# Kernel tuning notes

Measured on AMD Instinct MI355X. Metric: run time of the kernel, lower is better.

Reference implementation:

```python
import jax, jax.numpy as jnp
import numpy as np

D_MODEL = 1024
N_HEADS = 16
D_K = D_MODEL // N_HEADS
D_FF = 4096
EPS = 1e-5


def _linear_params(key, d_in, d_out):
    kw, kb = jax.random.split(key)
    lim = 1.0 / np.sqrt(d_in)
    W = jax.random.uniform(kw, (d_in, d_out), jnp.float32, -lim, lim)
    b = jax.random.uniform(kb, (d_out,), jnp.float32, -lim, lim)
    return W, b


def setup_inputs() -> dict:
    key = jax.random.key(0)
    ks = jax.random.split(key, 8)
    x = jax.random.normal(ks[0], (4, 2048, D_MODEL), jnp.float32)
    wq, bq = _linear_params(ks[1], D_MODEL, D_MODEL)
    wk, bk = _linear_params(ks[2], D_MODEL, D_MODEL)
    wv, bv = _linear_params(ks[3], D_MODEL, D_MODEL)
    wo, bo = _linear_params(ks[4], D_MODEL, D_MODEL)
    w1, b1 = _linear_params(ks[5], D_MODEL, D_FF)
    w2, b2 = _linear_params(ks[6], D_FF, D_MODEL)
    g1 = jnp.ones((D_MODEL,), jnp.float32)
    be1 = jnp.zeros((D_MODEL,), jnp.float32)
    g2 = jnp.ones((D_MODEL,), jnp.float32)
    be2 = jnp.zeros((D_MODEL,), jnp.float32)
    return dict(x=x, wq=wq, bq=bq, wk=wk, bk=bk, wv=wv, bv=bv, wo=wo, bo=bo,
                w1=w1, b1=b1, w2=w2, b2=b2, g1=g1, be1=be1, g2=g2, be2=be2)


def _layernorm(x, gamma, beta):
    mu = jnp.mean(x, axis=-1, keepdims=True)
    var = jnp.mean(jnp.square(x - mu), axis=-1, keepdims=True)
    return (x - mu) * jax.lax.rsqrt(var + EPS) * gamma + beta


def _encoder_layer(x, wq, bq, wk, bk, wv, bv, wo, bo, w1, b1, w2, b2, g1, be1, g2, be2):
    B, S, _ = x.shape
    # QKV projections, split into heads: (B, H, S, d_k)
    def split_heads(t):
        return t.reshape(B, S, N_HEADS, D_K).transpose(0, 2, 1, 3)
    q = split_heads(x @ wq + bq)
    k = split_heads(x @ wk + bk)
    v = split_heads(x @ wv + bv)
    scores = jnp.einsum('bhqd,bhkd->bhqk', q, k) / np.sqrt(D_K).astype(np.float32)
    attn = jax.nn.softmax(scores, axis=-1)
    ctx = jnp.einsum('bhqk,bhkd->bhqd', attn, v)
    ctx = ctx.transpose(0, 2, 1, 3).reshape(B, S, D_MODEL)
    attn_out = ctx @ wo + bo
    x = _layernorm(x + attn_out, g1, be1)
    ff = jax.nn.relu(x @ w1 + b1) @ w2 + b2
    x = _layernorm(x + ff, g2, be2)
    return x


def reference(x, wq, bq, wk, bk, wv, bv, wo, bo, w1, b1, w2, b2, g1, be1, g2, be2):
    return _encoder_layer(x, wq, bq, wk, bk, wv, bv, wo, bo, w1, b1, w2, b2, g1, be1, g2, be2)
```

## Files before the change

### kernel.cpp

```cpp
#include <hip/hip_runtime.h>
#include <hip/hip_bf16.h>

#define DEV __device__ __forceinline__

typedef __attribute__((ext_vector_type(8))) short bf16x8;
typedef __attribute__((ext_vector_type(4))) float f32x4;

constexpr int B = 4, S = 2048, D = 1024, H = 16, DK = 64, DFF = 4096;
constexpr int NT = B * S;
constexpr int HS = B * H * S;
constexpr float QSCALE = 0.125f * 1.44269504088896f;

#if __has_builtin(__builtin_amdgcn_exp2f)
#define EXP2(x) __builtin_amdgcn_exp2f(x)
#else
#define EXP2(x) exp2f(x)
#endif

#define BARRIER()                         \
  asm volatile("" ::: "memory");          \
  __builtin_amdgcn_s_barrier();           \
  asm volatile("" ::: "memory")

DEV unsigned short f2bf(float f) {
  return __builtin_bit_cast(unsigned short, __float2bfloat16(f));
}
DEV float bf2f(unsigned short u) { return __uint_as_float((unsigned)u << 16); }

DEV void gld16(unsigned short* ldsbase, const unsigned short* g, int lane) {
#if __has_builtin(__builtin_amdgcn_global_load_lds)
  __builtin_amdgcn_global_load_lds((const __attribute__((address_space(1))) unsigned int*)g,
                                   (__attribute__((address_space(3))) unsigned int*)ldsbase,
                                   16, 0, 0);
#else
  *(uint4*)(ldsbase + lane * 8) = *(const uint4*)g;
#endif
}

__global__ __launch_bounds__(256) void cvt_bf16_kernel(const float* __restrict__ in,
                                                       unsigned short* __restrict__ out, int n) {
  int i = (blockIdx.x * 256 + threadIdx.x) * 8;
  if (i >= n) return;
  float4 a = *(const float4*)(in + i);
  float4 b = *(const float4*)(in + i + 4);
  uint4 o;
  o.x = f2bf(a.x) | ((unsigned)f2bf(a.y) << 16);
  o.y = f2bf(a.z) | ((unsigned)f2bf(a.w) << 16);
  o.z = f2bf(b.x) | ((unsigned)f2bf(b.y) << 16);
  o.w = f2bf(b.z) | ((unsigned)f2bf(b.w) << 16);
  *(uint4*)(out + i) = o;
}

__global__ __launch_bounds__(256) void transpose_cvt_all_kernel(
    const float* __restrict__ wq, const float* __restrict__ wk, const float* __restrict__ wv,
    const float* __restrict__ wo, const float* __restrict__ w1, const float* __restrict__ w2,
    unsigned short* __restrict__ wqkvT, unsigned short* __restrict__ woT,
    unsigned short* __restrict__ w1T, unsigned short* __restrict__ w2T) {
  __shared__ unsigned short tile[64][72];
  int bid = blockIdx.x;
  const float* in;
  unsigned short* out;
  int R, C, tb;
  if (bid < 1024) {
    int wsel = bid >> 8;
    tb = bid & 255;
    R = 1024; C = 1024;
    in = wsel == 0 ? wq : wsel == 1 ? wk : wsel == 2 ? wv : wo;
    out = wsel < 3 ? wqkvT + (size_t)wsel * D * D : woT;
  } else if (bid < 2048) {
    tb = bid - 1024; R = 1024; C = 4096; in = w1; out = w1T;
  } else {
    tb = bid - 2048; R = 4096; C = 1024; in = w2; out = w2T;
  }
  int gx = C >> 6;
  int rb = (tb / gx) * 64, cb = (tb % gx) * 64;
  int t = threadIdx.x;
#pragma unroll
  for (int i = 0; i < 16; ++i) {
    int c = t + i * 256;
    int r = c >> 6, cc = c & 63;
    tile[cc][r] = f2bf(in[(size_t)(rb + r) * C + cb + cc]);
  }
  __syncthreads();
#pragma unroll
  for (int i = 0; i < 16; ++i) {
    int c = t + i * 256;
    int rr = c >> 6, cc = c & 63;
    out[(size_t)(cb + rr) * R + rb + cc] = tile[rr][cc];
  }
}

template <int BNW, int OMODE, bool RELU>
__global__ __launch_bounds__(512) void gemm256_kernel(const unsigned short* __restrict__ A,
                                                      const unsigned short* __restrict__ WT,
                                                      const float* __restrict__ bias0,
                                                      const float* __restrict__ bias1,
                                                      const float* __restrict__ bias2,
                                                      const unsigned short* __restrict__ res,
                                                      void* __restrict__ out0,
                                                      void* __restrict__ out1,
                                                      void* __restrict__ out2,
                                                      int M, int N, int K) {
  constexpr int BN = BNW * 64;
  __shared__ __align__(16) unsigned short sA[2][2][256 * 32];
  __shared__ __align__(16) unsigned short sB[2][2][BN * 32];

  int t = threadIdx.x, w = t >> 6, l = t & 63;
  int ll = l & 15, lh = l >> 4;

  int lin = blockIdx.x, nwg = gridDim.x;
  int wg = (nwg & 7) == 0 ? (lin & 7) * (nwg >> 3) + (lin >> 3) : lin;
  int gx = N / BN;
  int bn = wg % gx, bm = wg / gx;

  const int wm = (w >> 2) * 128, wn = (w & 3) * (BNW * 16);
  const int ua = (lh ^ ((ll >> 1) & 3)) * 8;

  f32x4 acc[8][BNW] = {};

  const int pr = t >> 2, up = t & 3;
  const int ulog = up ^ ((pr >> 1) & 3);
  const unsigned short* gA0 = A + ((size_t)bm * 256 + pr) * K + ulog * 8;
  const unsigned short* gB0 = WT + ((size_t)bn * BN + pr) * K + ulog * 8;

  auto stgA = [&](int buf, int kh, int tile) {
    const unsigned short* s = gA0 + (size_t)tile * 64 + kh * 32;
    gld16(&sA[buf][kh][w * 512], s, l);
    gld16(&sA[buf][kh][4096 + w * 512], s + (size_t)128 * K, l);
  };
  auto stgB = [&](int buf, int kh, int tile) {
    const unsigned short* s = gB0 + (size_t)tile * 64 + kh * 32;
    gld16(&sB[buf][kh][w * 512], s, l);
    if constexpr (BNW == 4) gld16(&sB[buf][kh][4096 + w * 512], s + (size_t)128 * K, l);
  };

  const int NK = K >> 6;
  stgA(0, 0, 0); stgB(0, 0, 0);
  stgA(0, 1, 0); stgB(0, 1, 0);
  stgA(1, 0, 1); stgB(1, 0, 1);
  if constexpr (BNW == 4) asm volatile("s_waitcnt vmcnt(4)" ::: "memory");
  else                    asm volatile("s_waitcnt vmcnt(3)" ::: "memory");
  BARRIER();

  bf16x8 bfr[BNW];
  for (int it = 0; it < NK; it += 2) {
    const bool more = it + 2 < NK;
#pragma unroll
    for (int ph = 0; ph < 8; ++ph) {
      const int tb = ph >> 2;
      const int kh = (ph >> 1) & 1;
      const int mq = ph & 1;
      bf16x8 af[4];
      if (mq == 0) {
#pragma unroll
        for (int nt = 0; nt < BNW; ++nt)
          bfr[nt] = *(const bf16x8*)(&sB[tb][kh][(wn + nt * 16 + ll) * 32 + ua]);
      }
#pragma unroll
      for (int i = 0; i < 4; ++i)
        af[i] = *(const bf16x8*)(&sA[tb][kh][(wm + (mq * 4 + i) * 16 + ll) * 32 + ua]);
      if (ph == 0) stgA(1, 1, it + 1);
      else if (ph == 1) stgB(1, 1, it + 1);
      else if (more) {
        if (ph == 2) stgA(0, 0, it + 2);
        else if (ph == 3) stgB(0, 0, it + 2);
        else if (ph == 4) stgA(0, 1, it + 2);
        else if (ph == 5) stgB(0, 1, it + 2);
        else if (ph == 6) stgA(1, 0, it + 3);
        else stgB(1, 0, it + 3);
      }
      BARRIER();
      __builtin_amdgcn_s_setprio(1);
#pragma unroll
      for (int i = 0; i < 4; ++i)
#pragma unroll
        for (int nt = 0; nt < BNW; ++nt)
          acc[mq * 4 + i][nt] =
              __builtin_amdgcn_mfma_f32_16x16x32_bf16(af[i], bfr[nt], acc[mq * 4 + i][nt], 0, 0, 0);
      __builtin_amdgcn_s_setprio(0);
      if (ph == 3 || ph == 7) {
        if (more) {
          if constexpr (BNW == 4) asm volatile("s_waitcnt vmcnt(4)" ::: "memory");
          else                    asm volatile("s_waitcnt vmcnt(3)" ::: "memory");
        } else {
          asm volatile("s_waitcnt vmcnt(0)" ::: "memory");
        }
      }
      BARRIER();
    }
  }

#pragma unroll
  for (int mt = 0; mt < 8; ++mt) {
#pragma unroll
    for (int nt = 0; nt < BNW; ++nt) {
      int col = bn * BN + wn + nt * 16 + ll;
      int row0 = bm * 256 + wm + mt * 16 + lh * 4;
      if constexpr (OMODE == 3) {
        int sec = col >> 10, c = col & 1023;
        float bv = (sec == 0 ? bias0 : (sec == 1 ? bias1 : bias2))[c];
        if (sec == 2) {
          int b_ = row0 >> 11, s_ = row0 & 2047;
          size_t vr = ((size_t)(b_ * H + (c >> 6)) * 64 + (c & 63)) * S + s_;
          uint2 pk;
          pk.x = (unsigned)f2bf(acc[mt][nt][0] + bv) | ((unsigned)f2bf(acc[mt][nt][1] + bv) << 16);
          pk.y = (unsigned)f2bf(acc[mt][nt][2] + bv) | ((unsigned)f2bf(acc[mt][nt][3] + bv) << 16);
          *(uint2*)((unsigned short*)out2 + vr) = pk;
        } else {
          unsigned short* o = sec == 0 ? (unsigned short*)out0 : (unsigned short*)out1;
          float sc_ = sec == 0 ? QSCALE : 1.f;
#pragma unroll
          for (int r = 0; r < 4; ++r)
            o[(size_t)(row0 + r) * 1024 + c] = f2bf((acc[mt][nt][r] + bv) * sc_);
        }
      } else {
        float bv = bias0[col];
#pragma unroll
        for (int r = 0; r < 4; ++r) {
          float v = acc[mt][nt][r] + bv;
          if (RELU) v = fmaxf(v, 0.f);
          if (OMODE == 4) {
            v += bf2f(res[(size_t)(row0 + r) * N + col]);
            ((unsigned short*)out0)[(size_t)(row0 + r) * N + col] = f2bf(v);
          } else if (OMODE == 1)
            ((unsigned short*)out0)[(size_t)(row0 + r) * N + col] = f2bf(v);
          else
            ((float*)out0)[(size_t)(row0 + r) * N + col] = v;
        }
      }
    }
  }
}

__global__ __launch_bounds__(512) void attn_kernel(const unsigned short* __restrict__ q,
                                                   const unsigned short* __restrict__ k,
                                                   const unsigned short* __restrict__ vt,
                                                   unsigned short* __restrict__ O1,
                                                   unsigned short* __restrict__ O2,
                                                   float* __restrict__ ml) {
  __shared__ __align__(16) unsigned short sK[2][64 * 64];
  __shared__ __align__(16) unsigned short sV[2][64 * 64];
  __shared__ __align__(16) unsigned short sP[8][16 * 72];
  int t = threadIdx.x, w = t >> 6, l = t & 63;
  int ll = l & 15, lh = l >> 4;
  int bh = blockIdx.y, hf = blockIdx.z;
  int q0 = blockIdx.x * 256 + w * 32;
  const size_t base = (size_t)(bh >> 4) * S * D + (size_t)(bh & 15) * DK;
  const size_t vtbase = (size_t)bh * 64 * S;
  unsigned short* Opart = hf ? O2 : O1;
  float* mlh = ml + (size_t)hf * 2 * HS;
  unsigned short* sPw = sP[w];

  const int srow = t >> 3;
  const int scol = 8 * ((t & 7) ^ (srow & 7));
  const unsigned short* gk = k + base + (size_t)srow * D + scol;
  const unsigned short* gv = vt + vtbase + (size_t)srow * S + scol;
  const int kb0 = hf * 1024;

  bf16x8 qf[2][2];
#pragma unroll
  for (int qs = 0; qs < 2; ++qs)
#pragma unroll
    for (int kk = 0; kk < 2; ++kk)
      qf[qs][kk] = *(const bf16x8*)(q + base + (size_t)(q0 + qs * 16 + ll) * D + kk * 32 + lh * 8);

  f32x4 cacc[2][4] = {};
  float m[2] = {-1e30f, -1e30f}, lsum[2] = {0.f, 0.f};

  const int swz = (ll & 7) << 3;

  gld16(&sK[0][w * 512], gk + (size_t)kb0 * D, l);
  gld16(&sV[0][w * 512], gv + kb0, l);
  asm volatile("s_waitcnt vmcnt(0)" ::: "memory");
  __syncthreads();

  int cur = 0;
  for (int step = 0; step < 16; ++step) {
    int kb = kb0 + step * 64;
    if (step < 15) {
      gld16(&sK[cur ^ 1][w * 512], gk + (size_t)(kb + 64) * D, l);
      gld16(&sV[cur ^ 1][w * 512], gv + (kb + 64), l);
    }
    const unsigned short* sKc = sK[cur];
    const unsigned short* sVc = sV[cur];

    bf16x8 kf[4][2];
#pragma unroll
    for (int nt = 0; nt < 4; ++nt)
#pragma unroll
      for (int kk = 0; kk < 2; ++kk)
        kf[nt][kk] = *(const bf16x8*)(sKc + (nt * 16 + ll) * 64 + ((kk * 32 + lh * 8) ^ swz));

    bf16x8 pf[2][2];
#pragma unroll
    for (int qs = 0; qs < 2; ++qs) {
      f32x4 sc[4] = {};
      __builtin_amdgcn_s_setprio(1);
#pragma unroll
      for (int nt = 0; nt < 4; ++nt) {
        sc[nt] = __builtin_amdgcn_mfma_f32_16x16x32_bf16(kf[nt][0], qf[qs][0], sc[nt], 0, 0, 0);
        sc[nt] = __builtin_amdgcn_mfma_f32_16x16x32_bf16(kf[nt][1], qf[qs][1], sc[nt], 0, 0, 0);
      }
      __builtin_amdgcn_s_setprio(0);
      float tm = -1e30f;
#pragma unroll
      for (int nt = 0; nt < 4; ++nt)
#pragma unroll
        for (int r = 0; r < 4; ++r) tm = fmaxf(tm, sc[nt][r]);
      tm = fmaxf(tm, __shfl_xor(tm, 16));
      tm = fmaxf(tm, __shfl_xor(tm, 32));
      if (!__all(tm <= m[qs] + 8.0f)) {
        float mn = fmaxf(m[qs], tm);
        float rsc = EXP2(m[qs] - mn);
        lsum[qs] *= rsc;
#pragma unroll
        for (int dt = 0; dt < 4; ++dt)
#pragma unroll
          for (int r = 0; r < 4; ++r) cacc[qs][dt][r] *= rsc;
        m[qs] = mn;
      }
      float p[4][4], ps = 0.f;
#pragma unroll
      for (int nt = 0; nt < 4; ++nt)
#pragma unroll
        for (int r = 0; r < 4; ++r) {
          p[nt][r] = EXP2(sc[nt][r] - m[qs]);
          ps += p[nt][r];
        }
      ps += __shfl_xor(ps, 16);
      ps += __shfl_xor(ps, 32);
      lsum[qs] += ps;
#pragma unroll
      for (int nt = 0; nt < 4; ++nt) {
        uint2 pk;
        pk.x = (unsigned)f2bf(p[nt][0]) | ((unsigned)f2bf(p[nt][1]) << 16);
        pk.y = (unsigned)f2bf(p[nt][2]) | ((unsigned)f2bf(p[nt][3]) << 16);
        *(uint2*)(&sPw[ll * 72 + nt * 16 + lh * 4]) = pk;
      }
      pf[qs][0] = *(const bf16x8*)(&sPw[ll * 72 + lh * 8]);
      pf[qs][1] = *(const bf16x8*)(&sPw[ll * 72 + 32 + lh * 8]);
    }

    bf16x8 vf[4][2];
#pragma unroll
    for (int dt = 0; dt < 4; ++dt)
#pragma unroll
      for (int kt = 0; kt < 2; ++kt)
        vf[dt][kt] = *(const bf16x8*)(sVc + (dt * 16 + ll) * 64 + ((kt * 32 + lh * 8) ^ swz));
    __builtin_amdgcn_s_setprio(1);
#pragma unroll
    for (int qs = 0; qs < 2; ++qs)
#pragma unroll
      for (int dt = 0; dt < 4; ++dt)
#pragma unroll
        for (int kt = 0; kt < 2; ++kt)
          cacc[qs][dt] = __builtin_amdgcn_mfma_f32_16x16x32_bf16(pf[qs][kt], vf[dt][kt], cacc[qs][dt], 0, 0, 0);
    __builtin_amdgcn_s_setprio(0);

    asm volatile("s_waitcnt vmcnt(0)" ::: "memory");
    __syncthreads();
    cur ^= 1;
  }

  int h64 = (bh & 15) * 64;
  int brow = (bh >> 4) * S;
#pragma unroll
  for (int qs = 0; qs < 2; ++qs) {
#pragma unroll
    for (int dt = 0; dt < 4; ++dt)
#pragma unroll
      for (int r = 0; r < 4; ++r) {
        int tok = brow + q0 + qs * 16 + lh * 4 + r;
        Opart[(size_t)tok * D + h64 + dt * 16 + ll] = f2bf(cacc[qs][dt][r]);
      }
    if (lh == 0) {
      int qq = q0 + qs * 16 + ll;
      mlh[(size_t)bh * S + qq] = m[qs];
      mlh[HS + (size_t)bh * S + qq] = lsum[qs];
    }
  }
}

__global__ __launch_bounds__(256) void attn_combine_kernel(const unsigned short* __restrict__ O1,
                                                           const unsigned short* __restrict__ O2,
                                                           const float* __restrict__ ml,
                                                           unsigned short* __restrict__ ctx) {
  int tok = blockIdx.x, tid = threadIdx.x;
  int h = tid >> 4;
  int bhs = ((tok >> 11) * H + h) * S + (tok & 2047);
  float m1 = ml[bhs], l1 = ml[HS + bhs];
  float m2 = ml[2 * HS + bhs], l2 = ml[3 * HS + bhs];
  float mm = fmaxf(m1, m2);
  float a1 = EXP2(m1 - mm), a2 = EXP2(m2 - mm);
  float inv = 1.f / (a1 * l1 + a2 * l2);
  a1 *= inv; a2 *= inv;
  size_t idx = (size_t)tok * D + tid * 4;
  ushort4 u1 = *(const ushort4*)(O1 + idx);
  ushort4 u2 = *(const ushort4*)(O2 + idx);
  uint2 pk;
  pk.x = (unsigned)f2bf(a1 * bf2f(u1.x) + a2 * bf2f(u2.x)) |
         ((unsigned)f2bf(a1 * bf2f(u1.y) + a2 * bf2f(u2.y)) << 16);
  pk.y = (unsigned)f2bf(a1 * bf2f(u1.z) + a2 * bf2f(u2.z)) |
         ((unsigned)f2bf(a1 * bf2f(u1.w) + a2 * bf2f(u2.w)) << 16);
  *(uint2*)(ctx + idx) = pk;
}

template <bool OUT_F32>
__global__ __launch_bounds__(256) void ln_kernel(const unsigned short* __restrict__ a,
                                                 const float* __restrict__ gamma,
                                                 const float* __restrict__ beta,
                                                 float* __restrict__ outf,
                                                 unsigned short* __restrict__ outb) {
  __shared__ float sred[8];
  size_t row = blockIdx.x;
  int t = threadIdx.x;
  size_t bidx = row * D + t * 4;
  ushort4 u = *(const ushort4*)(a + bidx);
  float4 x;
  x.x = bf2f(u.x); x.y = bf2f(u.y); x.z = bf2f(u.z); x.w = bf2f(u.w);

  float s = x.x + x.y + x.z + x.w;
#pragma unroll
  for (int msk = 32; msk; msk >>= 1) s += __shfl_xor(s, msk);
  if ((t & 63) == 0) sred[t >> 6] = s;
  __syncthreads();
  float mu = (sred[0] + sred[1] + sred[2] + sred[3]) * (1.f / D);

  float dx = x.x - mu, dy = x.y - mu, dz = x.z - mu, dw = x.w - mu;
  float sq = dx * dx + dy * dy + dz * dz + dw * dw;
#pragma unroll
  for (int msk = 32; msk; msk >>= 1) sq += __shfl_xor(sq, msk);
  __syncthreads();
  if ((t & 63) == 0) sred[t >> 6] = sq;
  __syncthreads();
  float var = (sred[0] + sred[1] + sred[2] + sred[3]) * (1.f / D);
  float rs = rsqrtf(var + 1e-5f);

  float4 g = *(const float4*)(gamma + t * 4);
  float4 be = *(const float4*)(beta + t * 4);
  float4 y;
  y.x = dx * rs * g.x + be.x;
  y.y = dy * rs * g.y + be.y;
  y.z = dz * rs * g.z + be.z;
  y.w = dw * rs * g.w + be.w;
  if (OUT_F32) {
    *(float4*)(outf + bidx) = y;
  } else {
    uint2 o;
    o.x = (unsigned)f2bf(y.x) | ((unsigned)f2bf(y.y) << 16);
    o.y = (unsigned)f2bf(y.z) | ((unsigned)f2bf(y.w) << 16);
    *(uint2*)(outb + bidx) = o;
  }
}

extern "C" void kernel_launch(void* const* d_in, const int* in_sizes, int n_in,
                              void* d_out, int out_size, void* d_ws, size_t ws_size,
                              hipStream_t stream) {
  const float* x   = (const float*)d_in[0];
  const float* wq  = (const float*)d_in[1];
  const float* bq  = (const float*)d_in[2];
  const float* wk  = (const float*)d_in[3];
  const float* bk  = (const float*)d_in[4];
  const float* wv  = (const float*)d_in[5];
  const float* bv  = (const float*)d_in[6];
  const float* wo  = (const float*)d_in[7];
  const float* bo  = (const float*)d_in[8];
  const float* w1  = (const float*)d_in[9];
  const float* b1  = (const float*)d_in[10];
  const float* w2  = (const float*)d_in[11];
  const float* b2  = (const float*)d_in[12];
  const float* g1  = (const float*)d_in[13];
  const float* be1 = (const float*)d_in[14];
  const float* g2  = (const float*)d_in[15];
  const float* be2 = (const float*)d_in[16];

  char* ws = (char*)d_ws;
  size_t off = 0;
  auto alloc = [&](size_t bytes) {
    char* p = ws + off;
    off += (bytes + 255) & ~(size_t)255;
    return p;
  };

  unsigned short* wqkvT = (unsigned short*)alloc((size_t)3 * D * D * 2);
  unsigned short* woT = (unsigned short*)alloc((size_t)D * D * 2);
  unsigned short* w1T = (unsigned short*)alloc((size_t)D * DFF * 2);
  unsigned short* w2T = (unsigned short*)alloc((size_t)DFF * D * 2);
  unsigned short* xb  = (unsigned short*)alloc((size_t)NT * D * 2);
  unsigned short* big = (unsigned short*)alloc((size_t)NT * DFF * 2);
  unsigned short* qb  = big;
  unsigned short* kb_ = big + (size_t)NT * D;
  unsigned short* ctb = big + (size_t)2 * NT * D;
  unsigned short* vtb = big + (size_t)3 * NT * D;
  unsigned short* O1  = (unsigned short*)alloc((size_t)NT * D * 2);
  unsigned short* O2  = (unsigned short*)alloc((size_t)NT * D * 2);
  float* mlbuf    = (float*)alloc((size_t)4 * HS * 4);
  unsigned short* x1b = xb;
  unsigned short* ffb = big;
  unsigned short* attn_out = O1;
  unsigned short* ff2 = O2;
  (void)ws_size; (void)in_sizes; (void)n_in; (void)out_size;

  cvt_bf16_kernel<<<NT * D / 2048, 256, 0, stream>>>(x, xb, NT * D);
  transpose_cvt_all_kernel<<<3072, 256, 0, stream>>>(wq, wk, wv, wo, w1, w2,
                                                     wqkvT, woT, w1T, w2T);

  gemm256_kernel<4, 3, false><<<(3 * D / 256) * (NT / 256), 512, 0, stream>>>(
      xb, wqkvT, bq, bk, bv, nullptr, qb, kb_, vtb, NT, 3 * D, D);

  attn_kernel<<<dim3(S / 256, B * H, 2), 512, 0, stream>>>(qb, kb_, vtb, O1, O2, mlbuf);
  attn_combine_kernel<<<NT, 256, 0, stream>>>(O1, O2, mlbuf, ctb);

  gemm256_kernel<2, 4, false><<<(D / 128) * (NT / 256), 512, 0, stream>>>(
      ctb, woT, bo, nullptr, nullptr, xb, attn_out, nullptr, nullptr, NT, D, D);

  ln_kernel<false><<<NT, 256, 0, stream>>>(attn_out, g1, be1, nullptr, x1b);

  gemm256_kernel<4, 1, true><<<(DFF / 256) * (NT / 256), 512, 0, stream>>>(
      x1b, w1T, b1, nullptr, nullptr, nullptr, ffb, nullptr, nullptr, NT, DFF, D);
  gemm256_kernel<2, 4, false><<<(D / 128) * (NT / 256), 512, 0, stream>>>(
      ffb, w2T, b2, nullptr, nullptr, x1b, ff2, nullptr, nullptr, NT, D, DFF);

  ln_kernel<true><<<NT, 256, 0, stream>>>(ff2, g2, be2, (float*)d_out, nullptr);
}
```

Before: 419.2 us.

## Drop split-KV attention and combine kernel; normalize in attention epilogue

```diff
diff --git a/kernel.cpp b/kernel.cpp
--- a/kernel.cpp
+++ b/kernel.cpp
@@ -8,7 +8,6 @@
 
 constexpr int B = 4, S = 2048, D = 1024, H = 16, DK = 64, DFF = 4096;
 constexpr int NT = B * S;
-constexpr int HS = B * H * S;
 constexpr float QSCALE = 0.125f * 1.44269504088896f;
 
 #if __has_builtin(__builtin_amdgcn_exp2f)
@@ -235,27 +234,22 @@
 __global__ __launch_bounds__(512) void attn_kernel(const unsigned short* __restrict__ q,
                                                    const unsigned short* __restrict__ k,
                                                    const unsigned short* __restrict__ vt,
-                                                   unsigned short* __restrict__ O1,
-                                                   unsigned short* __restrict__ O2,
-                                                   float* __restrict__ ml) {
+                                                   unsigned short* __restrict__ ctx) {
   __shared__ __align__(16) unsigned short sK[2][64 * 64];
   __shared__ __align__(16) unsigned short sV[2][64 * 64];
   __shared__ __align__(16) unsigned short sP[8][16 * 72];
   int t = threadIdx.x, w = t >> 6, l = t & 63;
   int ll = l & 15, lh = l >> 4;
-  int bh = blockIdx.y, hf = blockIdx.z;
+  int bh = blockIdx.y;
   int q0 = blockIdx.x * 256 + w * 32;
   const size_t base = (size_t)(bh >> 4) * S * D + (size_t)(bh & 15) * DK;
   const size_t vtbase = (size_t)bh * 64 * S;
-  unsigned short* Opart = hf ? O2 : O1;
-  float* mlh = ml + (size_t)hf * 2 * HS;
   unsigned short* sPw = sP[w];
 
   const int srow = t >> 3;
   const int scol = 8 * ((t & 7) ^ (srow & 7));
   const unsigned short* gk = k + base + (size_t)srow * D + scol;
   const unsigned short* gv = vt + vtbase + (size_t)srow * S + scol;
-  const int kb0 = hf * 1024;
 
   bf16x8 qf[2][2];
 #pragma unroll
@@ -269,15 +263,15 @@
 
   const int swz = (ll & 7) << 3;
 
-  gld16(&sK[0][w * 512], gk + (size_t)kb0 * D, l);
-  gld16(&sV[0][w * 512], gv + kb0, l);
+  gld16(&sK[0][w * 512], gk, l);
+  gld16(&sV[0][w * 512], gv, l);
   asm volatile("s_waitcnt vmcnt(0)" ::: "memory");
   __syncthreads();
 
   int cur = 0;
-  for (int step = 0; step < 16; ++step) {
-    int kb = kb0 + step * 64;
-    if (step < 15) {
+  for (int step = 0; step < 32; ++step) {
+    int kb = step * 64;
+    if (step < 31) {
       gld16(&sK[cur ^ 1][w * 512], gk + (size_t)(kb + 64) * D, l);
       gld16(&sV[cur ^ 1][w * 512], gv + (kb + 64), l);
     }
@@ -362,47 +356,20 @@
     cur ^= 1;
   }
 
-  int h64 = (bh & 15) * 64;
-  int brow = (bh >> 4) * S;
 #pragma unroll
   for (int qs = 0; qs < 2; ++qs) {
-#pragma unroll
-    for (int dt = 0; dt < 4; ++dt)
+    float inv[4];
+#pragma unroll
+    for (int r = 0; r < 4; ++r) inv[r] = 1.0f / __shfl(lsum[qs], lh * 4 + r);
+#pragma unroll
+    for (int dt = 0; dt < 4; ++dt) {
 #pragma unroll
       for (int r = 0; r < 4; ++r) {
-        int tok = brow + q0 + qs * 16 + lh * 4 + r;
-        Opart[(size_t)tok * D + h64 + dt * 16 + ll] = f2bf(cacc[qs][dt][r]);
-      }
-    if (lh == 0) {
-      int qq = q0 + qs * 16 + ll;
-      mlh[(size_t)bh * S + qq] = m[qs];
-      mlh[HS + (size_t)bh * S + qq] = lsum[qs];
+        int row = q0 + qs * 16 + lh * 4 + r;
+        ctx[base + (size_t)row * D + dt * 16 + ll] = f2bf(cacc[qs][dt][r] * inv[r]);
+      }
     }
   }
-}
-
-__global__ __launch_bounds__(256) void attn_combine_kernel(const unsigned short* __restrict__ O1,
-                                                           const unsigned short* __restrict__ O2,
-                                                           const float* __restrict__ ml,
-                                                           unsigned short* __restrict__ ctx) {
-  int tok = blockIdx.x, tid = threadIdx.x;
-  int h = tid >> 4;
-  int bhs = ((tok >> 11) * H + h) * S + (tok & 2047);
-  float m1 = ml[bhs], l1 = ml[HS + bhs];
-  float m2 = ml[2 * HS + bhs], l2 = ml[3 * HS + bhs];
-  float mm = fmaxf(m1, m2);
-  float a1 = EXP2(m1 - mm), a2 = EXP2(m2 - mm);
-  float inv = 1.f / (a1 * l1 + a2 * l2);
-  a1 *= inv; a2 *= inv;
-  size_t idx = (size_t)tok * D + tid * 4;
-  ushort4 u1 = *(const ushort4*)(O1 + idx);
-  ushort4 u2 = *(const ushort4*)(O2 + idx);
-  uint2 pk;
-  pk.x = (unsigned)f2bf(a1 * bf2f(u1.x) + a2 * bf2f(u2.x)) |
-         ((unsigned)f2bf(a1 * bf2f(u1.y) + a2 * bf2f(u2.y)) << 16);
-  pk.y = (unsigned)f2bf(a1 * bf2f(u1.z) + a2 * bf2f(u2.z)) |
-         ((unsigned)f2bf(a1 * bf2f(u1.w) + a2 * bf2f(u2.w)) << 16);
-  *(uint2*)(ctx + idx) = pk;
 }
 
 template <bool OUT_F32>
@@ -494,7 +461,6 @@
   unsigned short* vtb = big + (size_t)3 * NT * D;
   unsigned short* O1  = (unsigned short*)alloc((size_t)NT * D * 2);
   unsigned short* O2  = (unsigned short*)alloc((size_t)NT * D * 2);
-  float* mlbuf    = (float*)alloc((size_t)4 * HS * 4);
   unsigned short* x1b = xb;
   unsigned short* ffb = big;
   unsigned short* attn_out = O1;
@@ -508,8 +474,7 @@
   gemm256_kernel<4, 3, false><<<(3 * D / 256) * (NT / 256), 512, 0, stream>>>(
       xb, wqkvT, bq, bk, bv, nullptr, qb, kb_, vtb, NT, 3 * D, D);
 
-  attn_kernel<<<dim3(S / 256, B * H, 2), 512, 0, stream>>>(qb, kb_, vtb, O1, O2, mlbuf);
-  attn_combine_kernel<<<NT, 256, 0, stream>>>(O1, O2, mlbuf, ctb);
+  attn_kernel<<<dim3(S / 256, B * H), 512, 0, stream>>>(qb, kb_, vtb, ctb);
 
   gemm256_kernel<2, 4, false><<<(D / 128) * (NT / 256), 512, 0, stream>>>(
       ctb, woT, bo, nullptr, nullptr, xb, attn_out, nullptr, nullptr, NT, D, D);
```

Measured after the change: 404.1 us, median of 3. 1.04x faster.
